# Performance work log

Hardware: AMD Instinct MI355X
Metric: run time of the kernel (lower is better)

## Reference

```python
import jax, jax.numpy as jnp
import numpy as np
from jax import lax

EPS = 1e-5


def _conv(x, w, b, stride, pad):
    # x: [B,C,H,W], w: [O,I,kh,kw] (NCHW / OIHW, same as torch Conv2d)
    y = lax.conv_general_dilated(
        x, w, window_strides=stride,
        padding=[(pad[0], pad[0]), (pad[1], pad[1])],
        dimension_numbers=('NCHW', 'OIHW', 'NCHW'))
    return y + b[None, :, None, None]


def _bn(x, gamma, beta, mean, var):
    # BatchNorm2d in eval mode (running statistics)
    inv = gamma / jnp.sqrt(var + EPS)
    return x * inv[None, :, None, None] + (beta - mean * inv)[None, :, None, None]


def _mask_time(x, lens):
    # Vectorized replacement of the per-sample narrow/fill loop:
    # zero every time step >= lens[b] along the last axis.
    t = jnp.arange(x.shape[3])
    keep = (t[None, :] < lens[:, None]).astype(x.dtype)  # [B, W]
    return x * keep[:, None, None, :]


def _new_len(lens, kernel_w, stride_w, pad_w):
    # matches get_new_sequence_lengths for Conv2d with dilation 1
    return (lens + 2 * pad_w - (kernel_w - 1) - 1) // stride_w + 1


def _forward(inputs, seq_lengths,
             w1, b1, g1, be1, m1, v1,
             w2, b2, g2, be2, m2, v2):
    lens = seq_lengths.astype(jnp.int32)
    # layer 1: Conv2d(1,32,(41,11),(2,2),(20,5))
    x = _conv(inputs, w1, b1, (2, 2), (20, 5))
    lens = _new_len(lens, 11, 2, 5)
    x = _mask_time(x, lens)
    # BatchNorm2d(32) -> mask
    x = _mask_time(_bn(x, g1, be1, m1, v1), lens)
    # Hardtanh(0,20) -> mask
    x = _mask_time(jnp.clip(x, 0.0, 20.0), lens)
    # layer 2: Conv2d(32,32,(21,11),(2,1),(10,5))
    x = _conv(x, w2, b2, (2, 1), (10, 5))
    lens = _new_len(lens, 11, 1, 5)
    x = _mask_time(x, lens)
    x = _mask_time(_bn(x, g2, be2, m2, v2), lens)
    x = _mask_time(jnp.clip(x, 0.0, 20.0), lens)
    return x, lens


def setup_inputs() -> dict:
    key = jax.random.key(0)
    ks = jax.random.split(key, 8)
    inputs = jax.random.normal(ks[0], (32, 1, 161, 1024), dtype=jnp.float32)
    seq_lengths = jax.random.randint(ks[1], (32,), 1, 1024, dtype=jnp.int32)
    w1 = jax.random.normal(ks[2], (32, 1, 41, 11), dtype=jnp.float32) * 0.05
    b1 = jax.random.normal(ks[3], (32,), dtype=jnp.float32) * 0.05
    w2 = jax.random.normal(ks[4], (32, 32, 21, 11), dtype=jnp.float32) * 0.02
    b2 = jax.random.normal(ks[5], (32,), dtype=jnp.float32) * 0.05
    g1 = jnp.ones((32,), jnp.float32)
    be1 = jnp.zeros((32,), jnp.float32)
    m1 = jax.random.normal(ks[6], (32,), dtype=jnp.float32) * 0.1
    v1 = jnp.ones((32,), jnp.float32)
    g2 = jnp.ones((32,), jnp.float32)
    be2 = jnp.zeros((32,), jnp.float32)
    m2 = jax.random.normal(ks[7], (32,), dtype=jnp.float32) * 0.1
    v2 = jnp.ones((32,), jnp.float32)
    return {"inputs": inputs, "seq_lengths": seq_lengths,
            "w1": w1, "b1": b1, "g1": g1, "be1": be1, "m1": m1, "v1": v1,
            "w2": w2, "b2": b2, "g2": g2, "be2": be2, "m2": m2, "v2": v2}


def reference(inputs, seq_lengths, w1, b1, g1, be1, m1, v1,
              w2, b2, g2, be2, m2, v2):
    return _forward(inputs, seq_lengths, w1, b1, g1, be1, m1, v1,
                    w2, b2, g2, be2, m2, v2)
```

## Files before the change

kernel.cpp:

```cpp
#include <hip/hip_runtime.h>
#include <math.h>

#define B_    32
#define H_IN  161
#define W_IN  1024
#define C1_   32
#define H1_   81
#define W1_   512
#define C2_   32
#define H2_   41
#define W2_   512

#define OUT_X_SZ ((size_t)B_ * C2_ * H2_ * W2_)

#define WF2_B    0u
#define WF1_B    563200u
#define SCSH_B   609280u
#define LENS1_B  609792u
#define XG_B     609920u

#define WF2_N    281600
#define WF1_N    23040

typedef __bf16 v8bf __attribute__((ext_vector_type(8)));
typedef float v16f __attribute__((ext_vector_type(16)));

static __device__ __forceinline__ unsigned short f2bf(float f) {
    unsigned int u = __float_as_uint(f);
    unsigned int r = (u + 0x7fffu + ((u >> 16) & 1u)) >> 16;
    return (unsigned short)r;
}

__global__ void prep_kernel(const float* __restrict__ w1, const float* __restrict__ b1,
                            const float* __restrict__ g1, const float* __restrict__ be1,
                            const float* __restrict__ m1, const float* __restrict__ v1,
                            const float* __restrict__ w2, const float* __restrict__ b2,
                            const float* __restrict__ g2, const float* __restrict__ be2,
                            const float* __restrict__ m2, const float* __restrict__ v2,
                            const int* __restrict__ lens,
                            unsigned short* __restrict__ wf1, unsigned short* __restrict__ wf2,
                            float* __restrict__ scsh, int* __restrict__ lens1,
                            float* __restrict__ out_lens)
{
    const int i = blockIdx.x * blockDim.x + threadIdx.x;
    const int stride = gridDim.x * blockDim.x;

    for (int idx = i; idx < WF2_N; idx += stride) {
        int j  = idx & 7;
        int l  = (idx >> 3) & 63;
        int f  = idx >> 9;
        int ch = f & 1;
        int kwkh = f >> 1;
        int kw  = kwkh % 11;
        int khp = kwkh / 11;
        int kh  = khp - 2;
        int oc = l & 31;
        int c  = ch * 16 + ((l >> 5) << 3) + j;
        wf2[idx] = (kh >= 0 && kh < 21)
                 ? f2bf(w2[((oc * 32 + c) * 21 + kh) * 11 + kw]) : (unsigned short)0;
    }
    for (int idx = i; idx < WF1_N; idx += stride) {
        int j   = idx & 7;
        int l   = (idx >> 3) & 63;
        int khp = idx >> 9;
        int kh  = khp - 2;
        int k   = ((l >> 5) << 3) + j;
        int oc  = l & 31;
        wf1[idx] = (k < 11 && kh >= 0 && kh < 41)
                 ? f2bf(w1[oc * 451 + kh * 11 + k]) : (unsigned short)0;
    }
    if (i < 32) {
        float s1 = g1[i] / sqrtf(v1[i] + 1e-5f);
        scsh[i]      = s1;
        scsh[32 + i] = b1[i] * s1 + be1[i] - m1[i] * s1;
        float s2 = g2[i] / sqrtf(v2[i] + 1e-5f);
        scsh[64 + i] = s2;
        scsh[96 + i] = b2[i] * s2 + be2[i] - m2[i] * s2;
        int l1 = (lens[i] - 1) / 2 + 1;
        if (l1 > W1_) l1 = W1_;
        lens1[i] = l1;
        out_lens[i] = (float)l1;
    }
}

__global__ __launch_bounds__(256) void conv1_mfma(
    const float* __restrict__ x,
    const unsigned short* __restrict__ wf1,
    const float* __restrict__ scsh,
    const int* __restrict__ lens1,
    unsigned short* __restrict__ xg)
{
    const int t    = threadIdx.x;
    const int lane = t & 63;
    const int l31  = lane & 31;
    const int lhi  = lane >> 5;
    const int wv   = t >> 6;
    const int w0   = blockIdx.x * 256;
    const int hp   = blockIdx.y;
    const int b    = blockIdx.z;
    const int h0   = hp * 2;
    const bool h1ok = (h0 + 1) < H1_;

    __shared__ unsigned int srow[2][4][264];

    v16f acc[2][2];
#pragma unroll
    for (int hh = 0; hh < 2; ++hh)
#pragma unroll
        for (int nt = 0; nt < 2; ++nt)
#pragma unroll
            for (int q = 0; q < 16; ++q) acc[hh][nt][q] = 0.f;

    const int r0 = 2 * h0 - 20;
    const int cb = 2 * w0 - 5;
    const float* xb = x + (size_t)b * (H_IN * W_IN);

    const int dwbase = wv * 64 + l31 + 4 * lhi;

    {
        const int r = r0 + wv;
        const bool rok = (r >= 0) && (r < H_IN);
        const float* src = xb + (size_t)r * W_IN;
        unsigned int* drow = &srow[0][wv][0];
#pragma unroll
        for (int jj = 0; jj < 4; ++jj) {
            const int cp = lane + 64 * jj;
            const int c  = cb + 2 * cp;
            float a0 = 0.f, a1 = 0.f;
            if (rok) {
                if ((unsigned)c < (unsigned)W_IN)       a0 = src[c];
                if ((unsigned)(c + 1) < (unsigned)W_IN) a1 = src[c + 1];
            }
            drow[cp] = (unsigned int)f2bf(a0) | ((unsigned int)f2bf(a1) << 16);
        }
        if (lane < 8) {
            const int cp = 256 + lane;
            const int c  = cb + 2 * cp;
            float a0 = 0.f, a1 = 0.f;
            if (rok) {
                if ((unsigned)c < (unsigned)W_IN)       a0 = src[c];
                if ((unsigned)(c + 1) < (unsigned)W_IN) a1 = src[c + 1];
            }
            drow[cp] = (unsigned int)f2bf(a0) | ((unsigned int)f2bf(a1) << 16);
        }
    }
    __syncthreads();

    const uint4* wf1q = (const uint4*)wf1;

    for (int s = 0; s < 11; ++s) {
        const int p = s & 1;

        float sa[5][2];
#pragma unroll
        for (int jj = 0; jj < 5; ++jj) { sa[jj][0] = 0.f; sa[jj][1] = 0.f; }
        const int kpn = 4 * (s + 1) + wv;
        const int rn  = r0 + kpn;
        const bool sv = (s < 10) && (kpn < 43) && (rn >= 0) && (rn < H_IN);
        if (sv) {
            const float* src = xb + (size_t)rn * W_IN;
#pragma unroll
            for (int jj = 0; jj < 4; ++jj) {
                const int c = cb + 2 * (lane + 64 * jj);
                if ((unsigned)c < (unsigned)W_IN)       sa[jj][0] = src[c];
                if ((unsigned)(c + 1) < (unsigned)W_IN) sa[jj][1] = src[c + 1];
            }
            if (lane < 8) {
                const int c = cb + 2 * (256 + lane);
                if ((unsigned)c < (unsigned)W_IN)       sa[4][0] = src[c];
                if ((unsigned)(c + 1) < (unsigned)W_IN) sa[4][1] = src[c + 1];
            }
        }

#pragma unroll
        for (int j = 0; j < 4; ++j) {
            const int kp = 4 * s + j;
            if (kp > 42) break;
            const int r = r0 + kp;
            if (r >= 0 && r < H_IN) {
                uint4 a0u = wf1q[(kp + 2) * 32 + lane];
                uint4 a1u = wf1q[kp * 32 + lane];
                v8bf A0 = __builtin_bit_cast(v8bf, a0u);
                v8bf A1 = __builtin_bit_cast(v8bf, a1u);
                const unsigned int* bp = &srow[p][j][0];
                uint4 bu0, bu1;
                {
                    int dw = dwbase;
                    bu0.x = bp[dw]; bu0.y = bp[dw + 1]; bu0.z = bp[dw + 2]; bu0.w = bp[dw + 3];
                    dw += 32;
                    bu1.x = bp[dw]; bu1.y = bp[dw + 1]; bu1.z = bp[dw + 2]; bu1.w = bp[dw + 3];
                }
                v8bf B0 = __builtin_bit_cast(v8bf, bu0);
                v8bf B1 = __builtin_bit_cast(v8bf, bu1);
                acc[0][0] = __builtin_amdgcn_mfma_f32_32x32x16_bf16(A0, B0, acc[0][0], 0, 0, 0);
                acc[0][1] = __builtin_amdgcn_mfma_f32_32x32x16_bf16(A0, B1, acc[0][1], 0, 0, 0);
                acc[1][0] = __builtin_amdgcn_mfma_f32_32x32x16_bf16(A1, B0, acc[1][0], 0, 0, 0);
                acc[1][1] = __builtin_amdgcn_mfma_f32_32x32x16_bf16(A1, B1, acc[1][1], 0, 0, 0);
            }
        }

        if (sv) {
            unsigned int* drow = &srow[p ^ 1][wv][0];
#pragma unroll
            for (int jj = 0; jj < 4; ++jj)
                drow[lane + 64 * jj] =
                    (unsigned int)f2bf(sa[jj][0]) | ((unsigned int)f2bf(sa[jj][1]) << 16);
            if (lane < 8)
                drow[256 + lane] =
                    (unsigned int)f2bf(sa[4][0]) | ((unsigned int)f2bf(sa[4][1]) << 16);
        }
        __syncthreads();
    }

    const int l1 = lens1[b];
#pragma unroll
    for (int hh = 0; hh < 2; ++hh) {
        if (hh == 1 && !h1ok) break;
        const int h = h0 + hh;
#pragma unroll
        for (int nt = 0; nt < 2; ++nt) {
            const int w = w0 + wv * 64 + nt * 32 + l31;
            const bool keep = (w < l1);
            unsigned short* dp = xg + (((size_t)b * H1_ + h) * W1_ + w) * 32;
#pragma unroll
            for (int rq = 0; rq < 4; ++rq) {
                unsigned int wd[2];
#pragma unroll
                for (int d = 0; d < 2; ++d) {
                    int rg = rq * 4 + d * 2;
                    int oc = 8 * rq + 4 * lhi + d * 2;
                    float av0 = acc[hh][nt][rg];
                    float av1 = acc[hh][nt][rg + 1];
                    float v0 = fminf(fmaxf(fmaf(av0, scsh[oc],     scsh[32 + oc]), 0.f), 20.f);
                    float v1 = fminf(fmaxf(fmaf(av1, scsh[oc + 1], scsh[33 + oc]), 0.f), 20.f);
                    if (!keep) { v0 = 0.f; v1 = 0.f; }
                    wd[d] = (unsigned int)f2bf(v0) | ((unsigned int)f2bf(v1) << 16);
                }
                uint2 u; u.x = wd[0]; u.y = wd[1];
                *(uint2*)(dp + 8 * rq + 4 * lhi) = u;
            }
        }
    }
}

#define ROWB 21280

__global__ __launch_bounds__(256, 3) void conv2_mfma(
    const unsigned short* __restrict__ xg,
    const unsigned short* __restrict__ wf2,
    const float* __restrict__ scsh,
    const int* __restrict__ lens1,
    float* __restrict__ out)
{
    const int t    = threadIdx.x;
    const int lane = t & 63;
    const int l31  = lane & 31;
    const int lhi  = lane >> 5;
    const int wv   = t >> 6;

    const int id   = blockIdx.x;
    const int sid  = (id & 7) * 168 + (id >> 3);
    const int wblk = sid & 1;
    const int bh   = sid >> 1;
    const int hp   = bh % 21;
    const int b    = bh / 21;
    const int h0   = hp * 2;
    const bool h1ok = (h0 + 1) < H2_;
    const int w0B  = wblk << 8;

    __shared__ __align__(16) char sbuf[2 * ROWB];

    v16f acc[2][2];
#pragma unroll
    for (int hh = 0; hh < 2; ++hh)
#pragma unroll
        for (int nt = 0; nt < 2; ++nt)
#pragma unroll
            for (int q = 0; q < 16; ++q) acc[hh][nt][q] = 0.f;

    const int st_lds = (t >> 2) * 80 + (t & 3) * 16;
    const int rd_lds = (wv * 64 + l31) * 80 + lhi * 16;

    const unsigned short* xb = xg + (size_t)b * (H1_ * W1_ * 32);
    const int r0 = 2 * h0 - 10;

    {
        int r = r0;
        if (r >= 0 && r < H1_) {
            const unsigned short* xrow = xb + (size_t)r * (W1_ * 32);
#pragma unroll
            for (int it = 0; it < 5; ++it) {
                int i = t + it * 256;
                int wp = (i >> 2) + w0B - 5;
                uint4 z; z.x = z.y = z.z = z.w = 0u;
                if (i < 1064 && wp >= 0 && wp < W1_)
                    z = *(const uint4*)(xrow + (size_t)wp * 32 + (i & 3) * 8);
                if (i < 1064)
                    *(uint4*)(sbuf + st_lds + it * 5120) = z;
            }
        }
    }
    __syncthreads();

    const uint4* wq = (const uint4*)wf2;

    for (int kp = 0; kp < 23; ++kp) {
        const int p = kp & 1;
        const int rn = r0 + kp + 1;
        const bool stage_next = (kp < 22) && (rn >= 0) && (rn < H1_);

        uint4 g0, g1, g2, g3, g4;
        g0.x=g0.y=g0.z=g0.w=0u; g1=g0; g2=g0; g3=g0; g4=g0;
        if (stage_next) {
            const unsigned short* xrow = xb + (size_t)rn * (W1_ * 32);
            const int wbase = (t >> 2) + w0B - 5;
            const int ck = (t & 3) * 8;
            if (wbase >= 0 && wbase < W1_)                 g0 = *(const uint4*)(xrow + (size_t)wbase * 32 + ck);
            if (wbase + 64 >= 0 && wbase + 64 < W1_)       g1 = *(const uint4*)(xrow + (size_t)(wbase + 64) * 32 + ck);
            if (wbase + 128 < W1_)                         g2 = *(const uint4*)(xrow + (size_t)(wbase + 128) * 32 + ck);
            if (wbase + 192 < W1_)                         g3 = *(const uint4*)(xrow + (size_t)(wbase + 192) * 32 + ck);
            if (t < 40 && wbase + 256 < W1_)               g4 = *(const uint4*)(xrow + (size_t)(wbase + 256) * 32 + ck);
        }

        const int r = r0 + kp;
        if (r >= 0 && r < H1_) {
            const int f0 = (kp + 2) * 22;
            const int f1 = kp * 22;
            const char* bbase = sbuf + p * ROWB + rd_lds;
            __builtin_amdgcn_s_setprio(1);
#pragma unroll
            for (int kw = 0; kw < 11; ++kw) {
#pragma unroll
                for (int ch = 0; ch < 2; ++ch) {
                    uint4 a0u = wq[(f0 + kw * 2 + ch) * 64 + lane];
                    uint4 a1u = wq[(f1 + kw * 2 + ch) * 64 + lane];
                    uint4 b0u = *(const uint4*)(bbase + kw * 80 + ch * 32);
                    uint4 b1u = *(const uint4*)(bbase + 2560 + kw * 80 + ch * 32);
                    v8bf A0 = __builtin_bit_cast(v8bf, a0u);
                    v8bf A1 = __builtin_bit_cast(v8bf, a1u);
                    v8bf B0 = __builtin_bit_cast(v8bf, b0u);
                    v8bf B1 = __builtin_bit_cast(v8bf, b1u);
                    acc[0][0] = __builtin_amdgcn_mfma_f32_32x32x16_bf16(A0, B0, acc[0][0], 0, 0, 0);
                    acc[0][1] = __builtin_amdgcn_mfma_f32_32x32x16_bf16(A0, B1, acc[0][1], 0, 0, 0);
                    acc[1][0] = __builtin_amdgcn_mfma_f32_32x32x16_bf16(A1, B0, acc[1][0], 0, 0, 0);
                    acc[1][1] = __builtin_amdgcn_mfma_f32_32x32x16_bf16(A1, B1, acc[1][1], 0, 0, 0);
                }
            }
            __builtin_amdgcn_s_setprio(0);
        }

        if (stage_next) {
            char* wb = sbuf + (p ^ 1) * ROWB + st_lds;
            *(uint4*)(wb)            = g0;
            *(uint4*)(wb + 5120)     = g1;
            *(uint4*)(wb + 2 * 5120) = g2;
            *(uint4*)(wb + 3 * 5120) = g3;
            if (t < 40) *(uint4*)(wb + 4 * 5120) = g4;
        }
        __syncthreads();
    }

    const int l2 = lens1[b];
#pragma unroll
    for (int hh = 0; hh < 2; ++hh) {
        if (hh == 1 && !h1ok) break;
        const int h = h0 + hh;
#pragma unroll
        for (int nt = 0; nt < 2; ++nt) {
            const int w = w0B + wv * 64 + nt * 32 + l31;
            const bool keep = (w < l2);
#pragma unroll
            for (int reg = 0; reg < 16; ++reg) {
                const int oc = (reg & 3) + 8 * (reg >> 2) + 4 * lhi;
                float v = fmaf(acc[hh][nt][reg], scsh[64 + oc], scsh[96 + oc]);
                v = fminf(fmaxf(v, 0.f), 20.f);
                out[(((size_t)b * C2_ + oc) * H2_ + h) * W2_ + w] = keep ? v : 0.f;
            }
        }
    }
}

extern "C" void kernel_launch(void* const* d_in, const int* in_sizes, int n_in,
                              void* d_out, int out_size, void* d_ws, size_t ws_size,
                              hipStream_t stream) {
    const float* inputs = (const float*)d_in[0];
    const int*   slen   = (const int*)d_in[1];
    const float* w1 = (const float*)d_in[2];
    const float* b1 = (const float*)d_in[3];
    const float* g1 = (const float*)d_in[4];
    const float* be1 = (const float*)d_in[5];
    const float* m1 = (const float*)d_in[6];
    const float* v1 = (const float*)d_in[7];
    const float* w2 = (const float*)d_in[8];
    const float* b2 = (const float*)d_in[9];
    const float* g2 = (const float*)d_in[10];
    const float* be2 = (const float*)d_in[11];
    const float* m2 = (const float*)d_in[12];
    const float* v2 = (const float*)d_in[13];

    char* ws = (char*)d_ws;
    unsigned short* wf2  = (unsigned short*)(ws + WF2_B);
    unsigned short* wf1  = (unsigned short*)(ws + WF1_B);
    float*          scsh = (float*)(ws + SCSH_B);
    int*            lens1 = (int*)(ws + LENS1_B);
    unsigned short* xg   = (unsigned short*)(ws + XG_B);

    float* out_x    = (float*)d_out;
    float* out_lens = out_x + OUT_X_SZ;

    hipLaunchKernelGGL(prep_kernel, dim3(256), dim3(256), 0, stream,
                       w1, b1, g1, be1, m1, v1, w2, b2, g2, be2, m2, v2,
                       slen, wf1, wf2, scsh, lens1, out_lens);

    hipLaunchKernelGGL(conv1_mfma, dim3(2, 41, B_), dim3(256), 0, stream,
                       inputs, wf1, scsh, lens1, xg);

    hipLaunchKernelGGL(conv2_mfma, dim3(1344), dim3(256), 0, stream,
                       xg, wf2, scsh, lens1, out_x);
}
```

Before: 534.5 us.

## Halve conv2 block to two waves, each computing a 128-wide tile

Conv2 now runs 128 threads per block instead of 256. Each wave computes four 32-column tiles instead of two, so every A-fragment weight load feeds eight MFMAs rather than four, halving global weight traffic per output. The row staging loops are rewritten for the smaller thread count. In exchange, accumulator register pressure doubles and occupancy drops, and each thread issues more staging loads per row.

```diff
diff --git a/kernel.cpp b/kernel.cpp
--- a/kernel.cpp
+++ b/kernel.cpp
@@ -245,7 +245,7 @@
 
 #define ROWB 21280
 
-__global__ __launch_bounds__(256, 3) void conv2_mfma(
+__global__ __launch_bounds__(128, 2) void conv2_mfma(
     const unsigned short* __restrict__ xg,
     const unsigned short* __restrict__ wf2,
     const float* __restrict__ scsh,
@@ -256,7 +256,7 @@
     const int lane = t & 63;
     const int l31  = lane & 31;
     const int lhi  = lane >> 5;
-    const int wv   = t >> 6;
+    const int wid  = t >> 6;
 
     const int id   = blockIdx.x;
     const int sid  = (id & 7) * 168 + (id >> 3);
@@ -270,16 +270,16 @@
 
     __shared__ __align__(16) char sbuf[2 * ROWB];
 
-    v16f acc[2][2];
+    v16f acc[2][4];
 #pragma unroll
     for (int hh = 0; hh < 2; ++hh)
 #pragma unroll
-        for (int nt = 0; nt < 2; ++nt)
+        for (int nt = 0; nt < 4; ++nt)
 #pragma unroll
             for (int q = 0; q < 16; ++q) acc[hh][nt][q] = 0.f;
 
     const int st_lds = (t >> 2) * 80 + (t & 3) * 16;
-    const int rd_lds = (wv * 64 + l31) * 80 + lhi * 16;
+    const int rd_lds = (wid * 128 + l31) * 80 + lhi * 16;
 
     const unsigned short* xb = xg + (size_t)b * (H1_ * W1_ * 32);
     const int r0 = 2 * h0 - 10;
@@ -288,15 +288,16 @@
         int r = r0;
         if (r >= 0 && r < H1_) {
             const unsigned short* xrow = xb + (size_t)r * (W1_ * 32);
-#pragma unroll
-            for (int it = 0; it < 5; ++it) {
-                int i = t + it * 256;
-                int wp = (i >> 2) + w0B - 5;
+            const int wbase = (t >> 2) + w0B - 5;
+            const int ck = (t & 3) * 8;
+#pragma unroll
+            for (int it = 0; it < 9; ++it) {
+                if (it == 8 && t >= 40) break;
+                const int wp = wbase + it * 32;
                 uint4 z; z.x = z.y = z.z = z.w = 0u;
-                if (i < 1064 && wp >= 0 && wp < W1_)
-                    z = *(const uint4*)(xrow + (size_t)wp * 32 + (i & 3) * 8);
-                if (i < 1064)
-                    *(uint4*)(sbuf + st_lds + it * 5120) = z;
+                if (wp >= 0 && wp < W1_)
+                    z = *(const uint4*)(xrow + (size_t)wp * 32 + ck);
+                *(uint4*)(sbuf + st_lds + it * 2560) = z;
             }
         }
     }
@@ -309,17 +310,20 @@
         const int rn = r0 + kp + 1;
         const bool stage_next = (kp < 22) && (rn >= 0) && (rn < H1_);
 
-        uint4 g0, g1, g2, g3, g4;
-        g0.x=g0.y=g0.z=g0.w=0u; g1=g0; g2=g0; g3=g0; g4=g0;
+        uint4 g[9];
+#pragma unroll
+        for (int i = 0; i < 9; ++i) { g[i].x = g[i].y = g[i].z = g[i].w = 0u; }
         if (stage_next) {
             const unsigned short* xrow = xb + (size_t)rn * (W1_ * 32);
             const int wbase = (t >> 2) + w0B - 5;
             const int ck = (t & 3) * 8;
-            if (wbase >= 0 && wbase < W1_)                 g0 = *(const uint4*)(xrow + (size_t)wbase * 32 + ck);
-            if (wbase + 64 >= 0 && wbase + 64 < W1_)       g1 = *(const uint4*)(xrow + (size_t)(wbase + 64) * 32 + ck);
-            if (wbase + 128 < W1_)                         g2 = *(const uint4*)(xrow + (size_t)(wbase + 128) * 32 + ck);
-            if (wbase + 192 < W1_)                         g3 = *(const uint4*)(xrow + (size_t)(wbase + 192) * 32 + ck);
-            if (t < 40 && wbase + 256 < W1_)               g4 = *(const uint4*)(xrow + (size_t)(wbase + 256) * 32 + ck);
+#pragma unroll
+            for (int it = 0; it < 9; ++it) {
+                if (it == 8 && t >= 40) break;
+                const int wp = wbase + it * 32;
+                if (wp >= 0 && wp < W1_)
+                    g[it] = *(const uint4*)(xrow + (size_t)wp * 32 + ck);
+            }
         }
 
         const int r = r0 + kp;
@@ -334,16 +338,24 @@
                 for (int ch = 0; ch < 2; ++ch) {
                     uint4 a0u = wq[(f0 + kw * 2 + ch) * 64 + lane];
                     uint4 a1u = wq[(f1 + kw * 2 + ch) * 64 + lane];
+                    v8bf A0 = __builtin_bit_cast(v8bf, a0u);
+                    v8bf A1 = __builtin_bit_cast(v8bf, a1u);
                     uint4 b0u = *(const uint4*)(bbase + kw * 80 + ch * 32);
                     uint4 b1u = *(const uint4*)(bbase + 2560 + kw * 80 + ch * 32);
-                    v8bf A0 = __builtin_bit_cast(v8bf, a0u);
-                    v8bf A1 = __builtin_bit_cast(v8bf, a1u);
+                    uint4 b2u = *(const uint4*)(bbase + 5120 + kw * 80 + ch * 32);
+                    uint4 b3u = *(const uint4*)(bbase + 7680 + kw * 80 + ch * 32);
                     v8bf B0 = __builtin_bit_cast(v8bf, b0u);
                     v8bf B1 = __builtin_bit_cast(v8bf, b1u);
+                    v8bf B2 = __builtin_bit_cast(v8bf, b2u);
+                    v8bf B3 = __builtin_bit_cast(v8bf, b3u);
                     acc[0][0] = __builtin_amdgcn_mfma_f32_32x32x16_bf16(A0, B0, acc[0][0], 0, 0, 0);
                     acc[0][1] = __builtin_amdgcn_mfma_f32_32x32x16_bf16(A0, B1, acc[0][1], 0, 0, 0);
+                    acc[0][2] = __builtin_amdgcn_mfma_f32_32x32x16_bf16(A0, B2, acc[0][2], 0, 0, 0);
+                    acc[0][3] = __builtin_amdgcn_mfma_f32_32x32x16_bf16(A0, B3, acc[0][3], 0, 0, 0);
                     acc[1][0] = __builtin_amdgcn_mfma_f32_32x32x16_bf16(A1, B0, acc[1][0], 0, 0, 0);
                     acc[1][1] = __builtin_amdgcn_mfma_f32_32x32x16_bf16(A1, B1, acc[1][1], 0, 0, 0);
+                    acc[1][2] = __builtin_amdgcn_mfma_f32_32x32x16_bf16(A1, B2, acc[1][2], 0, 0, 0);
+                    acc[1][3] = __builtin_amdgcn_mfma_f32_32x32x16_bf16(A1, B3, acc[1][3], 0, 0, 0);
                 }
             }
             __builtin_amdgcn_s_setprio(0);
@@ -351,11 +363,11 @@
 
         if (stage_next) {
             char* wb = sbuf + (p ^ 1) * ROWB + st_lds;
-            *(uint4*)(wb)            = g0;
-            *(uint4*)(wb + 5120)     = g1;
-            *(uint4*)(wb + 2 * 5120) = g2;
-            *(uint4*)(wb + 3 * 5120) = g3;
-            if (t < 40) *(uint4*)(wb + 4 * 5120) = g4;
+#pragma unroll
+            for (int it = 0; it < 9; ++it) {
+                if (it == 8 && t >= 40) break;
+                *(uint4*)(wb + it * 2560) = g[it];
+            }
         }
         __syncthreads();
     }
@@ -366,8 +378,8 @@
         if (hh == 1 && !h1ok) break;
         const int h = h0 + hh;
 #pragma unroll
-        for (int nt = 0; nt < 2; ++nt) {
-            const int w = w0B + wv * 64 + nt * 32 + l31;
+        for (int nt = 0; nt < 4; ++nt) {
+            const int w = w0B + wid * 128 + nt * 32 + l31;
             const bool keep = (w < l2);
 #pragma unroll
             for (int reg = 0; reg < 16; ++reg) {
@@ -415,6 +427,6 @@
     hipLaunchKernelGGL(conv1_mfma, dim3(2, 41, B_), dim3(256), 0, stream,
                        inputs, wf1, scsh, lens1, xg);
 
-    hipLaunchKernelGGL(conv2_mfma, dim3(1344), dim3(256), 0, stream,
+    hipLaunchKernelGGL(conv2_mfma, dim3(1344), dim3(128), 0, stream,
                        xg, wf2, scsh, lens1, out_x);
 }
```

After: 573.1 us. +7.2%, slower.

## Warp-specialize conv2 with dedicated producer waves for LDS row staging

Applied to the files above, without the earlier changes.

Conv2 blocks grow from 256 to 384 threads. The two extra waves only load input rows from global memory into double-buffered LDS, while the four original waves only run MFMA and the epilogue, with both groups synchronised by block barriers each row. The aim is to take global-load latency and LDS store work off the compute waves' critical path. In exchange each block uses more threads and the barrier count is unchanged, and the launch bounds move to (384, 4), which could constrain registers for the accumulator-heavy compute waves.

```diff
diff --git a/kernel.cpp b/kernel.cpp
--- a/kernel.cpp
+++ b/kernel.cpp
@@ -245,7 +245,7 @@
 
 #define ROWB 21280
 
-__global__ __launch_bounds__(256, 3) void conv2_mfma(
+__global__ __launch_bounds__(384, 4) void conv2_mfma(
     const unsigned short* __restrict__ xg,
     const unsigned short* __restrict__ wf2,
     const float* __restrict__ scsh,
@@ -270,111 +270,119 @@
 
     __shared__ __align__(16) char sbuf[2 * ROWB];
 
-    v16f acc[2][2];
-#pragma unroll
-    for (int hh = 0; hh < 2; ++hh)
-#pragma unroll
-        for (int nt = 0; nt < 2; ++nt)
-#pragma unroll
-            for (int q = 0; q < 16; ++q) acc[hh][nt][q] = 0.f;
-
-    const int st_lds = (t >> 2) * 80 + (t & 3) * 16;
-    const int rd_lds = (wv * 64 + l31) * 80 + lhi * 16;
-
     const unsigned short* xb = xg + (size_t)b * (H1_ * W1_ * 32);
     const int r0 = 2 * h0 - 10;
 
-    {
-        int r = r0;
-        if (r >= 0 && r < H1_) {
-            const unsigned short* xrow = xb + (size_t)r * (W1_ * 32);
-#pragma unroll
-            for (int it = 0; it < 5; ++it) {
-                int i = t + it * 256;
-                int wp = (i >> 2) + w0B - 5;
+    if (wv >= 4) {
+        const int pt = t - 256;
+
+        if (r0 >= 0 && r0 < H1_) {
+            const char* xrow = (const char*)(xb + (size_t)r0 * (W1_ * 32));
+#pragma unroll
+            for (int i = 0; i < 9; ++i) {
+                const int c   = pt + 128 * i;
+                const int pos = c >> 2;
+                const int sg  = c & 3;
+                const int wp  = w0B + pos - 5;
                 uint4 z; z.x = z.y = z.z = z.w = 0u;
-                if (i < 1064 && wp >= 0 && wp < W1_)
-                    z = *(const uint4*)(xrow + (size_t)wp * 32 + (i & 3) * 8);
-                if (i < 1064)
-                    *(uint4*)(sbuf + st_lds + it * 5120) = z;
-            }
-        }
-    }
-    __syncthreads();
-
-    const uint4* wq = (const uint4*)wf2;
-
-    for (int kp = 0; kp < 23; ++kp) {
-        const int p = kp & 1;
-        const int rn = r0 + kp + 1;
-        const bool stage_next = (kp < 22) && (rn >= 0) && (rn < H1_);
-
-        uint4 g0, g1, g2, g3, g4;
-        g0.x=g0.y=g0.z=g0.w=0u; g1=g0; g2=g0; g3=g0; g4=g0;
-        if (stage_next) {
-            const unsigned short* xrow = xb + (size_t)rn * (W1_ * 32);
-            const int wbase = (t >> 2) + w0B - 5;
-            const int ck = (t & 3) * 8;
-            if (wbase >= 0 && wbase < W1_)                 g0 = *(const uint4*)(xrow + (size_t)wbase * 32 + ck);
-            if (wbase + 64 >= 0 && wbase + 64 < W1_)       g1 = *(const uint4*)(xrow + (size_t)(wbase + 64) * 32 + ck);
-            if (wbase + 128 < W1_)                         g2 = *(const uint4*)(xrow + (size_t)(wbase + 128) * 32 + ck);
-            if (wbase + 192 < W1_)                         g3 = *(const uint4*)(xrow + (size_t)(wbase + 192) * 32 + ck);
-            if (t < 40 && wbase + 256 < W1_)               g4 = *(const uint4*)(xrow + (size_t)(wbase + 256) * 32 + ck);
-        }
-
-        const int r = r0 + kp;
-        if (r >= 0 && r < H1_) {
-            const int f0 = (kp + 2) * 22;
-            const int f1 = kp * 22;
-            const char* bbase = sbuf + p * ROWB + rd_lds;
-            __builtin_amdgcn_s_setprio(1);
-#pragma unroll
-            for (int kw = 0; kw < 11; ++kw) {
-#pragma unroll
-                for (int ch = 0; ch < 2; ++ch) {
-                    uint4 a0u = wq[(f0 + kw * 2 + ch) * 64 + lane];
-                    uint4 a1u = wq[(f1 + kw * 2 + ch) * 64 + lane];
-                    uint4 b0u = *(const uint4*)(bbase + kw * 80 + ch * 32);
-                    uint4 b1u = *(const uint4*)(bbase + 2560 + kw * 80 + ch * 32);
-                    v8bf A0 = __builtin_bit_cast(v8bf, a0u);
-                    v8bf A1 = __builtin_bit_cast(v8bf, a1u);
-                    v8bf B0 = __builtin_bit_cast(v8bf, b0u);
-                    v8bf B1 = __builtin_bit_cast(v8bf, b1u);
-                    acc[0][0] = __builtin_amdgcn_mfma_f32_32x32x16_bf16(A0, B0, acc[0][0], 0, 0, 0);
-                    acc[0][1] = __builtin_amdgcn_mfma_f32_32x32x16_bf16(A0, B1, acc[0][1], 0, 0, 0);
-                    acc[1][0] = __builtin_amdgcn_mfma_f32_32x32x16_bf16(A1, B0, acc[1][0], 0, 0, 0);
-                    acc[1][1] = __builtin_amdgcn_mfma_f32_32x32x16_bf16(A1, B1, acc[1][1], 0, 0, 0);
-                }
-            }
-            __builtin_amdgcn_s_setprio(0);
-        }
-
-        if (stage_next) {
-            char* wb = sbuf + (p ^ 1) * ROWB + st_lds;
-            *(uint4*)(wb)            = g0;
-            *(uint4*)(wb + 5120)     = g1;
-            *(uint4*)(wb + 2 * 5120) = g2;
-            *(uint4*)(wb + 3 * 5120) = g3;
-            if (t < 40) *(uint4*)(wb + 4 * 5120) = g4;
+                if (c < 1064 && wp >= 0 && wp < W1_)
+                    z = *(const uint4*)(xrow + wp * 64 + sg * 16);
+                if (c < 1064)
+                    *(uint4*)(sbuf + pos * 80 + sg * 16) = z;
+            }
         }
         __syncthreads();
-    }
-
-    const int l2 = lens1[b];
-#pragma unroll
-    for (int hh = 0; hh < 2; ++hh) {
-        if (hh == 1 && !h1ok) break;
-        const int h = h0 + hh;
-#pragma unroll
-        for (int nt = 0; nt < 2; ++nt) {
-            const int w = w0B + wv * 64 + nt * 32 + l31;
-            const bool keep = (w < l2);
-#pragma unroll
-            for (int reg = 0; reg < 16; ++reg) {
-                const int oc = (reg & 3) + 8 * (reg >> 2) + 4 * lhi;
-                float v = fmaf(acc[hh][nt][reg], scsh[64 + oc], scsh[96 + oc]);
-                v = fminf(fmaxf(v, 0.f), 20.f);
-                out[(((size_t)b * C2_ + oc) * H2_ + h) * W2_ + w] = keep ? v : 0.f;
+
+        for (int kp = 0; kp < 23; ++kp) {
+            const int p  = kp & 1;
+            const int rn = r0 + kp + 1;
+            const bool sv = (kp < 22) && (rn >= 0) && (rn < H1_);
+            if (sv) {
+                const char* xrow = (const char*)(xb + (size_t)rn * (W1_ * 32));
+                uint4 g[9];
+#pragma unroll
+                for (int i = 0; i < 9; ++i) {
+                    const int c   = pt + 128 * i;
+                    const int pos = c >> 2;
+                    const int sg  = c & 3;
+                    const int wp  = w0B + pos - 5;
+                    g[i].x = g[i].y = g[i].z = g[i].w = 0u;
+                    if (c < 1064 && wp >= 0 && wp < W1_)
+                        g[i] = *(const uint4*)(xrow + wp * 64 + sg * 16);
+                }
+                char* db = sbuf + (p ^ 1) * ROWB;
+#pragma unroll
+                for (int i = 0; i < 9; ++i) {
+                    const int c   = pt + 128 * i;
+                    const int pos = c >> 2;
+                    const int sg  = c & 3;
+                    if (c < 1064)
+                        *(uint4*)(db + pos * 80 + sg * 16) = g[i];
+                }
+            }
+            __syncthreads();
+        }
+    } else {
+        v16f acc[2][2];
+#pragma unroll
+        for (int hh = 0; hh < 2; ++hh)
+#pragma unroll
+            for (int nt = 0; nt < 2; ++nt)
+#pragma unroll
+                for (int q = 0; q < 16; ++q) acc[hh][nt][q] = 0.f;
+
+        const int rd_lds = (wv * 64 + l31) * 80 + lhi * 16;
+        const uint4* wq  = (const uint4*)wf2;
+
+        __syncthreads();
+
+        for (int kp = 0; kp < 23; ++kp) {
+            const int p = kp & 1;
+            const int r = r0 + kp;
+            if (r >= 0 && r < H1_) {
+                const int f0 = (kp + 2) * 22;
+                const int f1 = kp * 22;
+                const char* bbase = sbuf + p * ROWB + rd_lds;
+                __builtin_amdgcn_s_setprio(1);
+#pragma unroll
+                for (int kw = 0; kw < 11; ++kw) {
+#pragma unroll
+                    for (int ch = 0; ch < 2; ++ch) {
+                        uint4 a0u = wq[(f0 + kw * 2 + ch) * 64 + lane];
+                        uint4 a1u = wq[(f1 + kw * 2 + ch) * 64 + lane];
+                        uint4 b0u = *(const uint4*)(bbase + kw * 80 + ch * 32);
+                        uint4 b1u = *(const uint4*)(bbase + 2560 + kw * 80 + ch * 32);
+                        v8bf A0 = __builtin_bit_cast(v8bf, a0u);
+                        v8bf A1 = __builtin_bit_cast(v8bf, a1u);
+                        v8bf B0 = __builtin_bit_cast(v8bf, b0u);
+                        v8bf B1 = __builtin_bit_cast(v8bf, b1u);
+                        acc[0][0] = __builtin_amdgcn_mfma_f32_32x32x16_bf16(A0, B0, acc[0][0], 0, 0, 0);
+                        acc[0][1] = __builtin_amdgcn_mfma_f32_32x32x16_bf16(A0, B1, acc[0][1], 0, 0, 0);
+                        acc[1][0] = __builtin_amdgcn_mfma_f32_32x32x16_bf16(A1, B0, acc[1][0], 0, 0, 0);
+                        acc[1][1] = __builtin_amdgcn_mfma_f32_32x32x16_bf16(A1, B1, acc[1][1], 0, 0, 0);
+                    }
+                }
+                __builtin_amdgcn_s_setprio(0);
+            }
+            __syncthreads();
+        }
+
+        const int l2 = lens1[b];
+#pragma unroll
+        for (int hh = 0; hh < 2; ++hh) {
+            if (hh == 1 && !h1ok) break;
+            const int h = h0 + hh;
+#pragma unroll
+            for (int nt = 0; nt < 2; ++nt) {
+                const int w = w0B + wv * 64 + nt * 32 + l31;
+                const bool keep = (w < l2);
+#pragma unroll
+                for (int reg = 0; reg < 16; ++reg) {
+                    const int oc = (reg & 3) + 8 * (reg >> 2) + 4 * lhi;
+                    float v = fmaf(acc[hh][nt][reg], scsh[64 + oc], scsh[96 + oc]);
+                    v = fminf(fmaxf(v, 0.f), 20.f);
+                    out[(((size_t)b * C2_ + oc) * H2_ + h) * W2_ + w] = keep ? v : 0.f;
+                }
             }
         }
     }
@@ -415,6 +423,6 @@
     hipLaunchKernelGGL(conv1_mfma, dim3(2, 41, B_), dim3(256), 0, stream,
                        inputs, wf1, scsh, lens1, xg);
 
-    hipLaunchKernelGGL(conv2_mfma, dim3(1344), dim3(256), 0, stream,
+    hipLaunchKernelGGL(conv2_mfma, dim3(1344), dim3(384), 0, stream,
                        xg, wf2, scsh, lens1, out_x);
 }
```

After: 541.7 us. About the same (+1.3%).
